# Performance work log

Measured on AMD Instinct MI355X. Metric: run time of the kernel, lower is better.

The kernel has to match this reference:

```python
import jax, jax.numpy as jnp
import numpy as np

N_NODES = 100000
N_HE = 20000
N_INC = 800000
D = 128
HEADS = 4
OUT = D // HEADS  # 32
NEG_SLOPE = 0.2
EPS_GN = 1e-5
EPS_SM = 1e-16


def graph_norm(x, w, b, ms):
    # PyG GraphNorm over a single graph: subtract learnable-scaled mean, normalize by std
    mean = jnp.mean(x, axis=0, keepdims=True)
    xc = x - ms * mean
    var = jnp.mean(xc * xc, axis=0, keepdims=True)
    return w * xc / jnp.sqrt(var + EPS_GN) + b


def frame_update(x, eidx, eattr, W, att, bias):
    # x: [N, D], eidx: [2, E] (row0 node ids, row1 hyperedge ids), eattr: [HE, D]
    xh = (x @ W).reshape(-1, HEADS, OUT)       # [N, H, O]
    eh = (eattr @ W).reshape(-1, HEADS, OUT)   # [HE, H, O]
    src = eidx[0]
    dst = eidx[1]
    x_i = xh[src]                              # [E, H, O] gathered node feats
    x_j = eh[dst]                              # [E, H, O] gathered hyperedge feats
    # attention logit: cat([x_i, x_j]) . att  summed over feature dim
    alpha = jnp.sum(x_i * att[:, :, :OUT], axis=-1) + jnp.sum(x_j * att[:, :, OUT:], axis=-1)  # [E, H]
    alpha = jnp.where(alpha >= 0, alpha, NEG_SLOPE * alpha)  # leaky_relu
    # segment softmax grouped by hyperedge id (dst), num_segments = N_HE
    m = jax.ops.segment_max(alpha, dst, num_segments=N_HE)   # [HE, H]
    ex = jnp.exp(alpha - m[dst])
    s = jax.ops.segment_sum(ex, dst, num_segments=N_HE)      # [HE, H]
    alpha = ex / (s[dst] + EPS_SM)                           # [E, H]
    # message = alpha * x_j where propagate's x_j = x[edge_index[0]] (node feats)
    msg = alpha[:, :, None] * x_i                            # [E, H, O]
    out = jax.ops.segment_sum(msg, dst, num_segments=N_HE)   # [HE, H, O]
    out = out.reshape(-1, HEADS * OUT)                       # concat heads
    return out + bias


def setup_inputs() -> dict:
    key = jax.random.key(0)
    ks = jax.random.split(key, 12)
    g = 1.0 / np.sqrt(D)
    inp = {
        "intra_x": jax.random.normal(ks[0], (N_NODES, D), jnp.float32),
        "intra_edge_attr": jax.random.normal(ks[1], (N_HE, D), jnp.float32),
        "inter_x": jax.random.normal(ks[2], (N_NODES, D), jnp.float32),
        "inter_edge_attr": jax.random.normal(ks[3], (N_HE, D), jnp.float32),
        "intra_edge_index": jnp.stack([
            jax.random.randint(ks[4], (N_INC,), 0, N_NODES),
            jax.random.randint(ks[5], (N_INC,), 0, N_HE)]).astype(jnp.int32),
        "inter_edge_index": jnp.stack([
            jax.random.randint(ks[6], (N_INC,), 0, N_NODES),
            jax.random.randint(ks[7], (N_INC,), 0, N_HE)]).astype(jnp.int32),
        "gn_intra_w": jnp.ones((D,), jnp.float32),
        "gn_intra_b": jnp.zeros((D,), jnp.float32),
        "gn_intra_ms": jnp.ones((D,), jnp.float32),
        "W_intra": jax.random.normal(ks[8], (D, HEADS * OUT), jnp.float32) * g,
        "att_intra": jax.random.normal(ks[9], (1, HEADS, 2 * OUT), jnp.float32) * g,
        "b_intra": jnp.zeros((HEADS * OUT,), jnp.float32),
        "gn_inter_w": jnp.ones((D,), jnp.float32),
        "gn_inter_b": jnp.zeros((D,), jnp.float32),
        "gn_inter_ms": jnp.ones((D,), jnp.float32),
        "W_inter": jax.random.normal(ks[10], (D, HEADS * OUT), jnp.float32) * g,
        "att_inter": jax.random.normal(ks[11], (1, HEADS, 2 * OUT), jnp.float32) * g,
        "b_inter": jnp.zeros((HEADS * OUT,), jnp.float32),
    }
    return inp


def reference(intra_x, intra_edge_index, intra_edge_attr,
              inter_x, inter_edge_index, inter_edge_attr,
              gn_intra_w, gn_intra_b, gn_intra_ms, W_intra, att_intra, b_intra,
              gn_inter_w, gn_inter_b, gn_inter_ms, W_inter, att_inter, b_inter):
    f_intra = frame_update(graph_norm(intra_x, gn_intra_w, gn_intra_b, gn_intra_ms),
                           intra_edge_index, intra_edge_attr, W_intra, att_intra, b_intra)
    f_inter = frame_update(graph_norm(inter_x, gn_inter_w, gn_inter_b, gn_inter_ms),
                           inter_edge_index, inter_edge_attr, W_inter, att_inter, b_inter)
    fusion = jnp.concatenate([
        jnp.mean(f_intra, axis=0),
        jnp.mean(f_inter, axis=0),
        jnp.mean(intra_x, axis=0),
        jnp.mean(inter_x, axis=0),
    ], axis=-1)  # [4*D]
    return fusion
```

## Files before the change

### kernel.cpp

```cpp
#include <hip/hip_runtime.h>

#define N_NODES 100000
#define N_HE    20000
#define N_EDGE  800000
#define DIM     128
#define NBS     98
#define NBD     40
#define CAP_S   9600
#define CAP_D   22500
#define SUBS    8
#define SUBD    16
#define PB      256
#define CHUNK   3125
#define STB     800
#define GPB     1024
#define GGRP    32

struct P {
  const void* x[2]; const void* ea[2]; const int* ei[2];
  const void* gw[2]; const void* gb[2]; const void* gms[2];
  const void* W[2]; const void* att[2]; const void* bias[2];
  float *stats, *a, *cw, *v, *u, *cst, *sPart, *wnPart, *gpart, *gpart2;
  unsigned *curS, *curD, *recS, *recD;
  unsigned short *lnb, *lhb, *hsv;
  unsigned short* xb;
  int useXb;
  int* flag; void* out;
};

__device__ __forceinline__ float ldf(const void* p, int i, int isbf){
  if (isbf){ unsigned short h = ((const unsigned short*)p)[i]; return __uint_as_float(((unsigned)h)<<16); }
  return ((const float*)p)[i];
}
__device__ __forceinline__ float b2f(unsigned short h){
  return __uint_as_float(((unsigned)h)<<16);
}
struct F8 { float v[8]; };
__device__ __forceinline__ F8 load8(const void* p, long idx, int isbf){
  F8 r;
  if (isbf){
    uint4 q = *(const uint4*)((const unsigned short*)p + idx);
    r.v[0]=__uint_as_float(q.x<<16); r.v[1]=__uint_as_float(q.x&0xFFFF0000u);
    r.v[2]=__uint_as_float(q.y<<16); r.v[3]=__uint_as_float(q.y&0xFFFF0000u);
    r.v[4]=__uint_as_float(q.z<<16); r.v[5]=__uint_as_float(q.z&0xFFFF0000u);
    r.v[6]=__uint_as_float(q.w<<16); r.v[7]=__uint_as_float(q.w&0xFFFF0000u);
  } else {
    const float4* q = (const float4*)((const float*)p + idx);
    float4 A=q[0], B=q[1];
    r.v[0]=A.x;r.v[1]=A.y;r.v[2]=A.z;r.v[3]=A.w;
    r.v[4]=B.x;r.v[5]=B.y;r.v[6]=B.z;r.v[7]=B.w;
  }
  return r;
}
__device__ __forceinline__ unsigned short f2bf(float f){
  unsigned u = __float_as_uint(f);
  return (unsigned short)((u + 0x7FFFu + ((u>>16)&1u)) >> 16);
}

__global__ void k_detect(P p){
  for (int i=threadIdx.x; i<872; i+=256) p.stats[i]=0.f;
  const unsigned* w = (const unsigned*)p.x[0];
  int bad = 0;
  for (int i = threadIdx.x; i < 4096; i += 256){
    float g = __uint_as_float(w[i]<<16);
    float ag = fabsf(g);
    if (!(ag==0.0f || (ag>1e-8f && ag<1e8f))) bad++;
  }
  for (int o=32;o;o>>=1) bad += __shfl_down(bad,o);
  __shared__ int sb;
  if (threadIdx.x==0) sb=0;
  __syncthreads();
  if ((threadIdx.x&63)==0) atomicAdd(&sb,bad);
  __syncthreads();
  if (threadIdx.x==0) *p.flag = (sb < 512) ? 1 : 0;
}

__global__ __launch_bounds__(256) void k_stats(P p){
  int f = blockIdx.y;
  const void* x = p.x[f];
  int isbf = *p.flag;
  int conv = (!isbf) && p.useXb;
  int cb = threadIdx.x & 15, rg = threadIdx.x >> 4;
  int rpb = (N_NODES + gridDim.x - 1)/gridDim.x;
  int r0 = blockIdx.x*rpb;
  int r1 = r0 + rpb; if (r1 > N_NODES) r1 = N_NODES;
  float s[8], q[8];
  #pragma unroll
  for (int j=0;j<8;j++){ s[j]=0.f; q[j]=0.f; }
  for (int r = r0 + rg; r < r1; r += 16){
    F8 xv = load8(x, (long)r*DIM + cb*8, isbf);
    #pragma unroll
    for (int j=0;j<8;j++){ s[j]+=xv.v[j]; q[j]+=xv.v[j]*xv.v[j]; }
    if (conv){
      uint4 o;
      o.x = (unsigned)f2bf(xv.v[0]) | ((unsigned)f2bf(xv.v[1])<<16);
      o.y = (unsigned)f2bf(xv.v[2]) | ((unsigned)f2bf(xv.v[3])<<16);
      o.z = (unsigned)f2bf(xv.v[4]) | ((unsigned)f2bf(xv.v[5])<<16);
      o.w = (unsigned)f2bf(xv.v[6]) | ((unsigned)f2bf(xv.v[7])<<16);
      *(uint4*)(p.xb + ((long)f*N_NODES + r)*DIM + cb*8) = o;
    }
  }
  __shared__ float red[256*9];
  #pragma unroll
  for (int j=0;j<8;j++) red[threadIdx.x*9+j]=s[j];
  __syncthreads();
  if (threadIdx.x < 128){
    int cb2 = threadIdx.x>>3, j = threadIdx.x&7;
    float a=0.f;
    for (int g=0; g<16; g++) a += red[(g*16+cb2)*9 + j];
    atomicAdd(&p.stats[f*256 + cb2*8 + j], a);
  }
  __syncthreads();
  #pragma unroll
  for (int j=0;j<8;j++) red[threadIdx.x*9+j]=q[j];
  __syncthreads();
  if (threadIdx.x < 128){
    int cb2 = threadIdx.x>>3, j = threadIdx.x&7;
    float a=0.f;
    for (int g=0; g<16; g++) a += red[(g*16+cb2)*9 + j];
    atomicAdd(&p.stats[f*256 + 128 + cb2*8 + j], a);
  }
}

__global__ void k_prep(P p){
  __shared__ float csh[2][128];
  int t = threadIdx.x;
  int isbf = *p.flag;
  int f = t>>7, d = t&127;
  float sum = p.stats[f*256+d], sq = p.stats[f*256+128+d];
  float mean = sum * (1.0f/N_NODES);
  float ms = ldf(p.gms[f], d, isbf);
  float gw = ldf(p.gw[f],  d, isbf);
  float gb = ldf(p.gb[f],  d, isbf);
  float var = sq*(1.0f/N_NODES) - (2.0f*ms - ms*ms)*mean*mean;
  float av = gw / sqrtf(var + 1e-5f);
  p.a[f*128+d] = av;
  csh[f][d] = gb - av*ms*mean;
  if (isbf) ((unsigned short*)p.out)[256 + f*128 + d] = f2bf(mean);
  else      ((float*)p.out)[256 + f*128 + d] = mean;
  #pragma unroll
  for (int h=0; h<4; h++){
    float w1=0.f, w2=0.f;
    for (int o=0;o<32;o++){
      float Wv = ldf(p.W[f], d*DIM + h*32 + o, isbf);
      w1 += Wv * ldf(p.att[f], h*64+o,    isbf);
      w2 += Wv * ldf(p.att[f], h*64+32+o, isbf);
    }
    p.v[f*512 + d*4 + h] = av*w1;
    p.u[f*512 + d*4 + h] = w2;
  }
  __syncthreads();
  float acc = 0.f;
  for (int dd=0; dd<128; dd++) acc += csh[f][dd]*ldf(p.W[f], dd*DIM+d, isbf);
  p.cw[f*128+d] = acc;
  __syncthreads();
  if (t < 8){
    int ff=t>>2, h=t&3;
    float s2=0.f;
    for (int o=0;o<32;o++) s2 += p.cw[ff*128+h*32+o]*ldf(p.att[ff], h*64+o, isbf);
    p.cst[ff*4+h]=s2;
  }
}

__global__ __launch_bounds__(256) void k_logits(P p){
  int job = blockIdx.y;
  int f = job & 1;
  bool node = job < 2;
  int isbf = *p.flag;
  const void* X; int xbf;
  if (node){
    if (isbf){ X = p.x[f]; xbf = 1; }
    else if (p.useXb){ X = p.xb + (long)f*N_NODES*DIM; xbf = 1; }
    else { X = p.x[f]; xbf = 0; }
  } else { X = p.ea[f]; xbf = isbf; }
  const float* coef = node ? (p.v + f*512) : (p.u + f*512);
  ushort4* outb = node ? ((ushort4*)p.lnb + (long)f*N_NODES)
                       : ((ushort4*)p.lhb + (long)f*N_HE);
  int R = node ? N_NODES : N_HE;
  int cb = threadIdx.x & 15, rl = threadIdx.x >> 4;
  float cf[8][4];
  #pragma unroll
  for (int j=0;j<8;j++)
    #pragma unroll
    for (int h=0;h<4;h++)
      cf[j][h] = coef[(cb*8+j)*4+h];
  float4 cst4 = make_float4(0.f,0.f,0.f,0.f);
  if (node) cst4 = *(const float4*)(p.cst + f*4);
  int rpb = (R + gridDim.x - 1)/gridDim.x;
  int r0 = blockIdx.x*rpb;
  int r1 = r0+rpb; if (r1>R) r1=R;
  for (int r = r0 + rl; r < r1; r += 16){
    F8 xv = load8(X, (long)r*DIM + cb*8, xbf);
    float a0=0.f,a1=0.f,a2=0.f,a3=0.f;
    #pragma unroll
    for (int j=0;j<8;j++){
      a0 += xv.v[j]*cf[j][0];
      a1 += xv.v[j]*cf[j][1];
      a2 += xv.v[j]*cf[j][2];
      a3 += xv.v[j]*cf[j][3];
    }
    #pragma unroll
    for (int m=1;m<16;m<<=1){
      a0 += __shfl_xor(a0,m);
      a1 += __shfl_xor(a1,m);
      a2 += __shfl_xor(a2,m);
      a3 += __shfl_xor(a3,m);
    }
    if (cb==0){
      ushort4 o;
      o.x = f2bf(a0 + cst4.x);
      o.y = f2bf(a1 + cst4.y);
      o.z = f2bf(a2 + cst4.z);
      o.w = f2bf(a3 + cst4.w);
      outb[r] = o;
    }
  }
}

__global__ __launch_bounds__(256) void k_bin(P p){
  __shared__ unsigned stage1[CHUNK];
  __shared__ unsigned stage2[CHUNK];
  __shared__ unsigned histS[NBS], histD[NBD];
  __shared__ unsigned startS[NBS], startD[NBD];
  __shared__ unsigned gbaseS[NBS], gbaseD[NBD];
  int b = blockIdx.x, f = blockIdx.y, t = threadIdx.x;
  const int* ei = p.ei[f];
  if (t < NBS) histS[t]=0;
  if (t < NBD) histD[t]=0;
  __syncthreads();
  int e0 = b*CHUNK;
  for (int i=t; i<CHUNK; i+=256){
    int src = ei[e0+i], dst = ei[N_EDGE+e0+i];
    unsigned nbs = (unsigned)src >> 10;
    stage1[i] = ((unsigned)src & 1023u) | ((unsigned)dst<<10) | (nbs<<25);
    atomicAdd(&histS[nbs], 1u);
    atomicAdd(&histD[(unsigned)dst>>9], 1u);
  }
  __syncthreads();
  if (t==0){ unsigned r=0; for (int k=0;k<NBS;k++){ startS[k]=r; r+=histS[k]; } }
  if (t==1){ unsigned r=0; for (int k=0;k<NBD;k++){ startD[k]=r; r+=histD[k]; } }
  __syncthreads();
  if (t < NBS) gbaseS[t] = atomicAdd(&p.curS[f*NBS+t], histS[t]);
  if (t >= 128 && t < 128+NBD) gbaseD[t-128] = atomicAdd(&p.curD[f*NBD+(t-128)], histD[t-128]);
  __syncthreads();
  if (t < NBS) histS[t]=0;
  __syncthreads();
  for (int i=t; i<CHUNK; i+=256){
    unsigned rec = stage1[i];
    unsigned nbs = rec>>25;
    unsigned r = atomicAdd(&histS[nbs],1u);
    stage2[startS[nbs]+r] = rec;
  }
  __syncthreads();
  for (int i=t; i<CHUNK; i+=256){
    unsigned rec = stage2[i];
    unsigned nbs = rec>>25;
    unsigned g = gbaseS[nbs] + (i - startS[nbs]);
    if (g < CAP_S) p.recS[((long)f*NBS+nbs)*CAP_S + g] = rec & 0x01FFFFFFu;
  }
  __syncthreads();
  if (t < NBD) histD[t]=0;
  __syncthreads();
  for (int i=t; i<CHUNK; i+=256){
    unsigned rec = stage1[i];
    unsigned dst = (rec>>10)&0x7FFFu;
    unsigned src = (rec>>25)*1024u + (rec&1023u);
    unsigned nbd = dst>>9;
    unsigned rd = (dst&511u) | (src<<9) | (nbd<<26);
    unsigned r = atomicAdd(&histD[nbd],1u);
    stage2[startD[nbd]+r] = rd;
  }
  __syncthreads();
  for (int i=t; i<CHUNK; i+=256){
    unsigned rd = stage2[i];
    unsigned nbd = rd>>26;
    unsigned g = gbaseD[nbd] + (i - startD[nbd]);
    if (g < CAP_D) p.recD[((long)f*NBD+nbd)*CAP_D + g] = rd & 0x03FFFFFFu;
  }
}

__global__ __launch_bounds__(256) void k_sD(P p){
  __shared__ float sh[512*4];
  int nbd = blockIdx.x, sub = blockIdx.y, f = blockIdx.z, t = threadIdx.x;
  for (int i=t; i<512; i+=256) *(float4*)(sh+i*4) = make_float4(0,0,0,0);
  __syncthreads();
  unsigned cnt = p.curD[f*NBD+nbd]; if (cnt > CAP_D) cnt = CAP_D;
  int lo = (int)((long)cnt*sub/SUBD), hi = (int)((long)cnt*(sub+1)/SUBD);
  const unsigned* base = p.recD + ((long)f*NBD+nbd)*CAP_D;
  const ushort4* lnb = (const ushort4*)p.lnb + (long)f*N_NODES;
  const ushort4* lhb = (const ushort4*)p.lhb + (long)f*N_HE;
  for (int i=lo+t; i<hi; i+=256){
    unsigned rd = base[i];
    unsigned dstRel = rd & 511u;
    unsigned src = rd >> 9;
    ushort4 A = lnb[src];
    ushort4 B = lhb[nbd*512 + dstRel];
    float z0=b2f(A.x)+b2f(B.x), z1=b2f(A.y)+b2f(B.y);
    float z2=b2f(A.z)+b2f(B.z), z3=b2f(A.w)+b2f(B.w);
    z0 = z0>=0.f? z0 : 0.2f*z0;  z1 = z1>=0.f? z1 : 0.2f*z1;
    z2 = z2>=0.f? z2 : 0.2f*z2;  z3 = z3>=0.f? z3 : 0.2f*z3;
    float* tgt = sh + dstRel*4;
    atomicAdd(tgt+0, __expf(z0));
    atomicAdd(tgt+1, __expf(z1));
    atomicAdd(tgt+2, __expf(z2));
    atomicAdd(tgt+3, __expf(z3));
  }
  __syncthreads();
  float* out = p.sPart + (((long)f*NBD+nbd)*SUBD + sub)*2048;
  for (int i=t; i<512; i+=256) *(float4*)(out+i*4) = *(float4*)(sh+i*4);
}

__global__ void k_sred(P p){
  int idx = blockIdx.x*256 + threadIdx.x;
  if (idx >= 2*N_HE) return;
  int f = idx / N_HE, he = idx % N_HE;
  int nbd = he>>9, rel = he&511;
  float4 acc = make_float4(0,0,0,0);
  const float* base = p.sPart + ((long)(f*NBD+nbd)*SUBD)*2048 + rel*4;
  #pragma unroll
  for (int s=0;s<SUBD;s++){
    float4 v = *(const float4*)(base + (long)s*2048);
    acc.x+=v.x; acc.y+=v.y; acc.z+=v.z; acc.w+=v.w;
  }
  ushort4 lh = ((const ushort4*)p.lhb)[(long)f*N_HE + he];
  uint4 o;
  o.x = (unsigned)lh.x | ((unsigned)lh.y<<16);
  o.y = (unsigned)lh.z | ((unsigned)lh.w<<16);
  o.z = (unsigned)f2bf(1.0f/(acc.x+1e-16f)) | ((unsigned)f2bf(1.0f/(acc.y+1e-16f))<<16);
  o.w = (unsigned)f2bf(1.0f/(acc.z+1e-16f)) | ((unsigned)f2bf(1.0f/(acc.w+1e-16f))<<16);
  ((uint4*)p.hsv)[(long)f*N_HE + he] = o;
}

__global__ __launch_bounds__(256) void k_wnD(P p){
  __shared__ float sh[1024*4];
  int nbs = blockIdx.x, sub = blockIdx.y, f = blockIdx.z, t = threadIdx.x;
  for (int i=t; i<1024; i+=256) *(float4*)(sh+i*4) = make_float4(0,0,0,0);
  __syncthreads();
  unsigned cnt = p.curS[f*NBS+nbs]; if (cnt > CAP_S) cnt = CAP_S;
  int lo = (int)((long)cnt*sub/SUBS), hi = (int)((long)cnt*(sub+1)/SUBS);
  const unsigned* base = p.recS + ((long)f*NBS+nbs)*CAP_S;
  const ushort4* lnb = (const ushort4*)p.lnb + (long)f*N_NODES;
  const uint4* hsv = (const uint4*)p.hsv + (long)f*N_HE;
  for (int i=lo+t; i<hi; i+=256){
    unsigned rec = base[i];
    unsigned srcRel = rec & 1023u;
    unsigned dst = rec >> 10;
    ushort4 A = lnb[nbs*1024 + srcRel];
    uint4 H = hsv[dst];
    float z0=b2f(A.x)+b2f((unsigned short)(H.x&0xFFFF)), z1=b2f(A.y)+b2f((unsigned short)(H.x>>16));
    float z2=b2f(A.z)+b2f((unsigned short)(H.y&0xFFFF)), z3=b2f(A.w)+b2f((unsigned short)(H.y>>16));
    z0 = z0>=0.f? z0 : 0.2f*z0;  z1 = z1>=0.f? z1 : 0.2f*z1;
    z2 = z2>=0.f? z2 : 0.2f*z2;  z3 = z3>=0.f? z3 : 0.2f*z3;
    float si0=b2f((unsigned short)(H.z&0xFFFF)), si1=b2f((unsigned short)(H.z>>16));
    float si2=b2f((unsigned short)(H.w&0xFFFF)), si3=b2f((unsigned short)(H.w>>16));
    float* tgt = sh + srcRel*4;
    atomicAdd(tgt+0, __expf(z0)*si0);
    atomicAdd(tgt+1, __expf(z1)*si1);
    atomicAdd(tgt+2, __expf(z2)*si2);
    atomicAdd(tgt+3, __expf(z3)*si3);
  }
  __syncthreads();
  float* out = p.wnPart + (((long)f*NBS+nbs)*SUBS + sub)*4096;
  for (int i=t; i<1024; i+=256) *(float4*)(out+i*4) = *(float4*)(sh+i*4);
}

__global__ __launch_bounds__(256) void k_gpass(P p){
  int f = blockIdx.y;
  int isbf = *p.flag;
  const void* xs; int xbf;
  if (isbf){ xs = p.x[f]; xbf = 1; }
  else if (p.useXb){ xs = p.xb + (long)f*N_NODES*DIM; xbf = 1; }
  else { xs = p.x[f]; xbf = 0; }
  int cb = threadIdx.x & 15, rg = threadIdx.x >> 4;
  float acc[8][4]; float sw[4]={0.f,0.f,0.f,0.f};
  #pragma unroll
  for (int j=0;j<8;j++)
    #pragma unroll
    for (int h=0;h<4;h++) acc[j][h]=0.f;
  int rpb = (N_NODES + gridDim.x - 1)/gridDim.x;
  int r0 = blockIdx.x*rpb;
  int r1 = r0+rpb; if (r1>N_NODES) r1=N_NODES;
  for (int r = r0 + rg; r < r1; r += 16){
    int nbs = r>>10, rel = r&1023;
    const float* wb = p.wnPart + ((long)(f*NBS+nbs)*SUBS)*4096 + rel*4;
    float4 wv = make_float4(0,0,0,0);
    #pragma unroll
    for (int s=0;s<SUBS;s++){
      float4 v = *(const float4*)(wb + (long)s*4096);
      wv.x+=v.x; wv.y+=v.y; wv.z+=v.z; wv.w+=v.w;
    }
    F8 xv = load8(xs, (long)r*DIM + cb*8, xbf);
    float wvv[4]={wv.x,wv.y,wv.z,wv.w};
    #pragma unroll
    for (int j=0;j<8;j++)
      #pragma unroll
      for (int h=0;h<4;h++) acc[j][h] += xv.v[j]*wvv[h];
    if (cb==0){ sw[0]+=wv.x; sw[1]+=wv.y; sw[2]+=wv.z; sw[3]+=wv.w; }
  }
  __shared__ float red[16][16][33];
  __shared__ float red2[16][4];
  #pragma unroll
  for (int j=0;j<8;j++)
    #pragma unroll
    for (int h=0;h<4;h++) red[rg][cb][j*4+h]=acc[j][h];
  if (cb==0){ red2[rg][0]=sw[0]; red2[rg][1]=sw[1]; red2[rg][2]=sw[2]; red2[rg][3]=sw[3]; }
  __syncthreads();
  float* gp = p.gpart + ((long)f*GPB + blockIdx.x)*520;
  for (int idx=threadIdx.x; idx<512; idx+=256){
    int d=idx>>2, h=idx&3, cb2=d>>3, j=d&7;
    float a=0.f;
    #pragma unroll
    for (int g=0; g<16; g++) a += red[g][cb2][j*4+h];
    gp[idx] = a;
  }
  if (threadIdx.x<4){
    float a=0.f;
    for (int g=0;g<16;g++) a+=red2[g][threadIdx.x];
    gp[512+threadIdx.x] = a;
  }
}

__global__ void k_gredA(P p){
  int g = blockIdx.x, f = blockIdx.y;
  int slabs = GPB/GGRP;
  const float* base = p.gpart + ((long)f*GPB + (long)g*slabs)*520;
  for (int i=threadIdx.x; i<516; i+=256){
    float acc = 0.f;
    for (int s=0;s<slabs;s++) acc += base[(long)s*520 + i];
    p.gpart2[((long)f*GGRP + g)*520 + i] = acc;
  }
}

__global__ void k_final(P p){
  __shared__ float Gs[2][512];
  __shared__ float SWs[2][4];
  int t = threadIdx.x;
  for (int idx=t; idx<2*516; idx+=256){
    int f = idx/516, i = idx%516;
    const float* b = p.gpart2 + (long)f*GGRP*520 + i;
    float acc = 0.f;
    for (int g=0; g<GGRP; g++) acc += b[(long)g*520];
    if (i < 512) Gs[f][i] = acc; else SWs[f][i-512] = acc;
  }
  __syncthreads();
  int isbf = *p.flag;
  int f = t>>7, k = t&127, h = k>>5;
  float acc = 0.f;
  for (int d=0; d<128; d++)
    acc += Gs[f][d*4+h] * p.a[f*128+d] * ldf(p.W[f], d*DIM+k, isbf);
  acc += p.cw[f*128+k]*SWs[f][h];
  float o = acc*(1.0f/N_HE) + ldf(p.bias[f], k, isbf);
  if (isbf) ((unsigned short*)p.out)[f*128+k] = f2bf(o);
  else      ((float*)p.out)[f*128+k] = o;
}

extern "C" void kernel_launch(void* const* d_in, const int* in_sizes, int n_in,
                              void* d_out, int out_size, void* d_ws, size_t ws_size,
                              hipStream_t stream){
  P p;
  p.x[0]=d_in[0];  p.ea[0]=d_in[1];  p.x[1]=d_in[2];  p.ea[1]=d_in[3];
  p.ei[0]=(const int*)d_in[4];  p.ei[1]=(const int*)d_in[5];
  p.gw[0]=d_in[6];  p.gb[0]=d_in[7];  p.gms[0]=d_in[8];
  p.W[0]=d_in[9];   p.att[0]=d_in[10]; p.bias[0]=d_in[11];
  p.gw[1]=d_in[12]; p.gb[1]=d_in[13]; p.gms[1]=d_in[14];
  p.W[1]=d_in[15];  p.att[1]=d_in[16]; p.bias[1]=d_in[17];

  float* w = (float*)d_ws;
  size_t off = 0;
  p.stats = w+off; off += 512;
  p.flag  = (int*)(w+off); off += 8;
  p.curS  = (unsigned*)(w+off); off += 256;
  p.curD  = (unsigned*)(w+off); off += 96;
  p.a     = w+off; off += 256;
  p.cw    = w+off; off += 256;
  p.v     = w+off; off += 1024;
  p.u     = w+off; off += 1024;
  p.cst   = w+off; off += 16;
  p.lnb   = (unsigned short*)(w+off); off += (size_t)2*N_NODES*2;
  p.lhb   = (unsigned short*)(w+off); off += (size_t)2*N_HE*2;
  p.hsv   = (unsigned short*)(w+off); off += (size_t)2*N_HE*4;
  p.recS  = (unsigned*)(w+off); off += (size_t)2*NBS*CAP_S;
  p.recD  = (unsigned*)(w+off); off += (size_t)2*NBD*CAP_D;
  p.sPart = w+off; off += (size_t)2*NBD*SUBD*2048;
  p.wnPart= w+off; off += (size_t)2*NBS*SUBS*4096;
  p.gpart = w+off; off += (size_t)2*GPB*520;
  p.gpart2= w+off; off += (size_t)2*GGRP*520;
  p.xb    = (unsigned short*)(w+off);
  size_t tot_with_xb = off + (size_t)2*N_NODES*DIM/2;
  p.useXb = (tot_with_xb*sizeof(float) <= ws_size) ? 1 : 0;
  p.out   = d_out;

  k_detect <<<dim3(1),          dim3(256), 0, stream>>>(p);
  k_stats  <<<dim3(STB,2),      dim3(256), 0, stream>>>(p);
  k_prep   <<<dim3(1),          dim3(256), 0, stream>>>(p);
  k_logits <<<dim3(STB,4),      dim3(256), 0, stream>>>(p);
  k_bin    <<<dim3(PB,2),       dim3(256), 0, stream>>>(p);
  k_sD     <<<dim3(NBD,SUBD,2), dim3(256), 0, stream>>>(p);
  k_sred   <<<dim3((2*N_HE+255)/256), dim3(256), 0, stream>>>(p);
  k_wnD    <<<dim3(NBS,SUBS,2), dim3(256), 0, stream>>>(p);
  k_gpass  <<<dim3(GPB,2),      dim3(256), 0, stream>>>(p);
  k_gredA  <<<dim3(GGRP,2),     dim3(256), 0, stream>>>(p);
  k_final  <<<dim3(1),          dim3(256), 0, stream>>>(p);
}
```

Before: 252.9 us.

## Merge stats and binning kernels, drop bf16 copy of x, fuse final reduction

Fuses the graph-norm statistics pass and the edge binning pass into a single launch, with blocks split by blockIdx.y and sharing one shared-memory buffer. Removes the bf16 staging copy of the node features, so the logits and gather passes read the original fp32 inputs directly. Merges the last reduction with the final projection using a last-block-done atomic counter, and halves the grid sizes for the stats/logits and gather passes. This saves launches and the bf16 write traffic, at the cost of doubled fp32 read traffic in the later passes.

```diff
diff --git a/kernel.cpp b/kernel.cpp
--- a/kernel.cpp
+++ b/kernel.cpp
@@ -12,8 +12,8 @@
 #define SUBD    16
 #define PB      256
 #define CHUNK   3125
-#define STB     800
-#define GPB     1024
+#define STB     400
+#define GPB     512
 #define GGRP    32
 
 struct P {
@@ -21,10 +21,8 @@
   const void* gw[2]; const void* gb[2]; const void* gms[2];
   const void* W[2]; const void* att[2]; const void* bias[2];
   float *stats, *a, *cw, *v, *u, *cst, *sPart, *wnPart, *gpart, *gpart2;
-  unsigned *curS, *curD, *recS, *recD;
+  unsigned *curS, *curD, *recS, *recD, *done;
   unsigned short *lnb, *lhb, *hsv;
-  unsigned short* xb;
-  int useXb;
   int* flag; void* out;
 };
 
@@ -58,7 +56,7 @@
 }
 
 __global__ void k_detect(P p){
-  for (int i=threadIdx.x; i<872; i+=256) p.stats[i]=0.f;
+  for (int i=threadIdx.x; i<880; i+=256) p.stats[i]=0.f;
   const unsigned* w = (const unsigned*)p.x[0];
   int bad = 0;
   for (int i = threadIdx.x; i < 4096; i += 256){
@@ -75,50 +73,109 @@
   if (threadIdx.x==0) *p.flag = (sb < 512) ? 1 : 0;
 }
 
-__global__ __launch_bounds__(256) void k_stats(P p){
-  int f = blockIdx.y;
-  const void* x = p.x[f];
-  int isbf = *p.flag;
-  int conv = (!isbf) && p.useXb;
-  int cb = threadIdx.x & 15, rg = threadIdx.x >> 4;
-  int rpb = (N_NODES + gridDim.x - 1)/gridDim.x;
-  int r0 = blockIdx.x*rpb;
-  int r1 = r0 + rpb; if (r1 > N_NODES) r1 = N_NODES;
-  float s[8], q[8];
-  #pragma unroll
-  for (int j=0;j<8;j++){ s[j]=0.f; q[j]=0.f; }
-  for (int r = r0 + rg; r < r1; r += 16){
-    F8 xv = load8(x, (long)r*DIM + cb*8, isbf);
-    #pragma unroll
-    for (int j=0;j<8;j++){ s[j]+=xv.v[j]; q[j]+=xv.v[j]*xv.v[j]; }
-    if (conv){
-      uint4 o;
-      o.x = (unsigned)f2bf(xv.v[0]) | ((unsigned)f2bf(xv.v[1])<<16);
-      o.y = (unsigned)f2bf(xv.v[2]) | ((unsigned)f2bf(xv.v[3])<<16);
-      o.z = (unsigned)f2bf(xv.v[4]) | ((unsigned)f2bf(xv.v[5])<<16);
-      o.w = (unsigned)f2bf(xv.v[6]) | ((unsigned)f2bf(xv.v[7])<<16);
-      *(uint4*)(p.xb + ((long)f*N_NODES + r)*DIM + cb*8) = o;
-    }
-  }
-  __shared__ float red[256*9];
-  #pragma unroll
-  for (int j=0;j<8;j++) red[threadIdx.x*9+j]=s[j];
-  __syncthreads();
-  if (threadIdx.x < 128){
-    int cb2 = threadIdx.x>>3, j = threadIdx.x&7;
-    float a=0.f;
-    for (int g=0; g<16; g++) a += red[(g*16+cb2)*9 + j];
-    atomicAdd(&p.stats[f*256 + cb2*8 + j], a);
-  }
-  __syncthreads();
-  #pragma unroll
-  for (int j=0;j<8;j++) red[threadIdx.x*9+j]=q[j];
-  __syncthreads();
-  if (threadIdx.x < 128){
-    int cb2 = threadIdx.x>>3, j = threadIdx.x&7;
-    float a=0.f;
-    for (int g=0; g<16; g++) a += red[(g*16+cb2)*9 + j];
-    atomicAdd(&p.stats[f*256 + 128 + cb2*8 + j], a);
+__global__ __launch_bounds__(256) void k_statsbin(P p){
+  __shared__ unsigned smem[6664];
+  int t = threadIdx.x;
+  if (blockIdx.y < 2){
+    int f = blockIdx.y;
+    const void* x = p.x[f];
+    int isbf = *p.flag;
+    int cb = t & 15, rg = t >> 4;
+    int rpb = (N_NODES + STB - 1)/STB;
+    int r0 = blockIdx.x*rpb;
+    int r1 = r0 + rpb; if (r1 > N_NODES) r1 = N_NODES;
+    float s[8], q[8];
+    #pragma unroll
+    for (int j=0;j<8;j++){ s[j]=0.f; q[j]=0.f; }
+    for (int r = r0 + rg; r < r1; r += 16){
+      F8 xv = load8(x, (long)r*DIM + cb*8, isbf);
+      #pragma unroll
+      for (int j=0;j<8;j++){ s[j]+=xv.v[j]; q[j]+=xv.v[j]*xv.v[j]; }
+    }
+    float* red = (float*)smem;
+    #pragma unroll
+    for (int j=0;j<8;j++) red[t*9+j]=s[j];
+    __syncthreads();
+    if (t < 128){
+      int cb2 = t>>3, j = t&7;
+      float a=0.f;
+      for (int g=0; g<16; g++) a += red[(g*16+cb2)*9 + j];
+      atomicAdd(&p.stats[f*256 + cb2*8 + j], a);
+    }
+    __syncthreads();
+    #pragma unroll
+    for (int j=0;j<8;j++) red[t*9+j]=q[j];
+    __syncthreads();
+    if (t < 128){
+      int cb2 = t>>3, j = t&7;
+      float a=0.f;
+      for (int g=0; g<16; g++) a += red[(g*16+cb2)*9 + j];
+      atomicAdd(&p.stats[f*256 + 128 + cb2*8 + j], a);
+    }
+    return;
+  }
+  int b = blockIdx.x, f = blockIdx.y - 2;
+  if (b >= PB) return;
+  unsigned* stage1 = smem;
+  unsigned* stage2 = smem + 3125;
+  unsigned* histS  = smem + 6250;
+  unsigned* histD  = smem + 6348;
+  unsigned* startS = smem + 6388;
+  unsigned* startD = smem + 6486;
+  unsigned* gbaseS = smem + 6526;
+  unsigned* gbaseD = smem + 6624;
+  const int* ei = p.ei[f];
+  if (t < NBS) histS[t]=0;
+  if (t < NBD) histD[t]=0;
+  __syncthreads();
+  int e0 = b*CHUNK;
+  for (int i=t; i<CHUNK; i+=256){
+    int src = ei[e0+i], dst = ei[N_EDGE+e0+i];
+    unsigned nbs = (unsigned)src >> 10;
+    stage1[i] = ((unsigned)src & 1023u) | ((unsigned)dst<<10) | (nbs<<25);
+    atomicAdd(&histS[nbs], 1u);
+    atomicAdd(&histD[(unsigned)dst>>9], 1u);
+  }
+  __syncthreads();
+  if (t==0){ unsigned r=0; for (int k=0;k<NBS;k++){ startS[k]=r; r+=histS[k]; } }
+  if (t==1){ unsigned r=0; for (int k=0;k<NBD;k++){ startD[k]=r; r+=histD[k]; } }
+  __syncthreads();
+  if (t < NBS) gbaseS[t] = atomicAdd(&p.curS[f*NBS+t], histS[t]);
+  if (t >= 128 && t < 128+NBD) gbaseD[t-128] = atomicAdd(&p.curD[f*NBD+(t-128)], histD[t-128]);
+  __syncthreads();
+  if (t < NBS) histS[t]=0;
+  __syncthreads();
+  for (int i=t; i<CHUNK; i+=256){
+    unsigned rec = stage1[i];
+    unsigned nbs = rec>>25;
+    unsigned r = atomicAdd(&histS[nbs],1u);
+    stage2[startS[nbs]+r] = rec;
+  }
+  __syncthreads();
+  for (int i=t; i<CHUNK; i+=256){
+    unsigned rec = stage2[i];
+    unsigned nbs = rec>>25;
+    unsigned g = gbaseS[nbs] + (i - startS[nbs]);
+    if (g < CAP_S) p.recS[((long)f*NBS+nbs)*CAP_S + g] = rec & 0x01FFFFFFu;
+  }
+  __syncthreads();
+  if (t < NBD) histD[t]=0;
+  __syncthreads();
+  for (int i=t; i<CHUNK; i+=256){
+    unsigned rec = stage1[i];
+    unsigned dst = (rec>>10)&0x7FFFu;
+    unsigned src = (rec>>25)*1024u + (rec&1023u);
+    unsigned nbd = dst>>9;
+    unsigned rd = (dst&511u) | (src<<9) | (nbd<<26);
+    unsigned r = atomicAdd(&histD[nbd],1u);
+    stage2[startD[nbd]+r] = rd;
+  }
+  __syncthreads();
+  for (int i=t; i<CHUNK; i+=256){
+    unsigned rd = stage2[i];
+    unsigned nbd = rd>>26;
+    unsigned g = gbaseD[nbd] + (i - startD[nbd]);
+    if (g < CAP_D) p.recD[((long)f*NBD+nbd)*CAP_D + g] = rd & 0x03FFFFFFu;
   }
 }
 
@@ -167,12 +224,7 @@
   int f = job & 1;
   bool node = job < 2;
   int isbf = *p.flag;
-  const void* X; int xbf;
-  if (node){
-    if (isbf){ X = p.x[f]; xbf = 1; }
-    else if (p.useXb){ X = p.xb + (long)f*N_NODES*DIM; xbf = 1; }
-    else { X = p.x[f]; xbf = 0; }
-  } else { X = p.ea[f]; xbf = isbf; }
+  const void* X = node ? p.x[f] : p.ea[f];
   const float* coef = node ? (p.v + f*512) : (p.u + f*512);
   ushort4* outb = node ? ((ushort4*)p.lnb + (long)f*N_NODES)
                        : ((ushort4*)p.lhb + (long)f*N_HE);
@@ -190,7 +242,7 @@
   int r0 = blockIdx.x*rpb;
   int r1 = r0+rpb; if (r1>R) r1=R;
   for (int r = r0 + rl; r < r1; r += 16){
-    F8 xv = load8(X, (long)r*DIM + cb*8, xbf);
+    F8 xv = load8(X, (long)r*DIM + cb*8, isbf);
     float a0=0.f,a1=0.f,a2=0.f,a3=0.f;
     #pragma unroll
     for (int j=0;j<8;j++){
@@ -214,68 +266,6 @@
       o.w = f2bf(a3 + cst4.w);
       outb[r] = o;
     }
-  }
-}
-
-__global__ __launch_bounds__(256) void k_bin(P p){
-  __shared__ unsigned stage1[CHUNK];
-  __shared__ unsigned stage2[CHUNK];
-  __shared__ unsigned histS[NBS], histD[NBD];
-  __shared__ unsigned startS[NBS], startD[NBD];
-  __shared__ unsigned gbaseS[NBS], gbaseD[NBD];
-  int b = blockIdx.x, f = blockIdx.y, t = threadIdx.x;
-  const int* ei = p.ei[f];
-  if (t < NBS) histS[t]=0;
-  if (t < NBD) histD[t]=0;
-  __syncthreads();
-  int e0 = b*CHUNK;
-  for (int i=t; i<CHUNK; i+=256){
-    int src = ei[e0+i], dst = ei[N_EDGE+e0+i];
-    unsigned nbs = (unsigned)src >> 10;
-    stage1[i] = ((unsigned)src & 1023u) | ((unsigned)dst<<10) | (nbs<<25);
-    atomicAdd(&histS[nbs], 1u);
-    atomicAdd(&histD[(unsigned)dst>>9], 1u);
-  }
-  __syncthreads();
-  if (t==0){ unsigned r=0; for (int k=0;k<NBS;k++){ startS[k]=r; r+=histS[k]; } }
-  if (t==1){ unsigned r=0; for (int k=0;k<NBD;k++){ startD[k]=r; r+=histD[k]; } }
-  __syncthreads();
-  if (t < NBS) gbaseS[t] = atomicAdd(&p.curS[f*NBS+t], histS[t]);
-  if (t >= 128 && t < 128+NBD) gbaseD[t-128] = atomicAdd(&p.curD[f*NBD+(t-128)], histD[t-128]);
-  __syncthreads();
-  if (t < NBS) histS[t]=0;
-  __syncthreads();
-  for (int i=t; i<CHUNK; i+=256){
-    unsigned rec = stage1[i];
-    unsigned nbs = rec>>25;
-    unsigned r = atomicAdd(&histS[nbs],1u);
-    stage2[startS[nbs]+r] = rec;
-  }
-  __syncthreads();
-  for (int i=t; i<CHUNK; i+=256){
-    unsigned rec = stage2[i];
-    unsigned nbs = rec>>25;
-    unsigned g = gbaseS[nbs] + (i - startS[nbs]);
-    if (g < CAP_S) p.recS[((long)f*NBS+nbs)*CAP_S + g] = rec & 0x01FFFFFFu;
-  }
-  __syncthreads();
-  if (t < NBD) histD[t]=0;
-  __syncthreads();
-  for (int i=t; i<CHUNK; i+=256){
-    unsigned rec = stage1[i];
-    unsigned dst = (rec>>10)&0x7FFFu;
-    unsigned src = (rec>>25)*1024u + (rec&1023u);
-    unsigned nbd = dst>>9;
-    unsigned rd = (dst&511u) | (src<<9) | (nbd<<26);
-    unsigned r = atomicAdd(&histD[nbd],1u);
-    stage2[startD[nbd]+r] = rd;
-  }
-  __syncthreads();
-  for (int i=t; i<CHUNK; i+=256){
-    unsigned rd = stage2[i];
-    unsigned nbd = rd>>26;
-    unsigned g = gbaseD[nbd] + (i - startD[nbd]);
-    if (g < CAP_D) p.recD[((long)f*NBD+nbd)*CAP_D + g] = rd & 0x03FFFFFFu;
   }
 }
 
@@ -367,10 +357,7 @@
 __global__ __launch_bounds__(256) void k_gpass(P p){
   int f = blockIdx.y;
   int isbf = *p.flag;
-  const void* xs; int xbf;
-  if (isbf){ xs = p.x[f]; xbf = 1; }
-  else if (p.useXb){ xs = p.xb + (long)f*N_NODES*DIM; xbf = 1; }
-  else { xs = p.x[f]; xbf = 0; }
+  const void* xs = p.x[f];
   int cb = threadIdx.x & 15, rg = threadIdx.x >> 4;
   float acc[8][4]; float sw[4]={0.f,0.f,0.f,0.f};
   #pragma unroll
@@ -389,7 +376,7 @@
       float4 v = *(const float4*)(wb + (long)s*4096);
       wv.x+=v.x; wv.y+=v.y; wv.z+=v.z; wv.w+=v.w;
     }
-    F8 xv = load8(xs, (long)r*DIM + cb*8, xbf);
+    F8 xv = load8(xs, (long)r*DIM + cb*8, isbf);
     float wvv[4]={wv.x,wv.y,wv.z,wv.w};
     #pragma unroll
     for (int j=0;j<8;j++)
@@ -420,7 +407,7 @@
   }
 }
 
-__global__ void k_gredA(P p){
+__global__ void k_gredfin(P p){
   int g = blockIdx.x, f = blockIdx.y;
   int slabs = GPB/GGRP;
   const float* base = p.gpart + ((long)f*GPB + (long)g*slabs)*520;
@@ -429,29 +416,36 @@
     for (int s=0;s<slabs;s++) acc += base[(long)s*520 + i];
     p.gpart2[((long)f*GGRP + g)*520 + i] = acc;
   }
-}
-
-__global__ void k_final(P p){
+  __syncthreads();
+  __threadfence();
+  __shared__ unsigned isLast;
+  if (threadIdx.x==0){
+    unsigned old = atomicAdd(p.done, 1u);
+    isLast = (old == (unsigned)(GGRP*2 - 1)) ? 1u : 0u;
+  }
+  __syncthreads();
+  if (!isLast) return;
+  __threadfence();
   __shared__ float Gs[2][512];
   __shared__ float SWs[2][4];
   int t = threadIdx.x;
   for (int idx=t; idx<2*516; idx+=256){
-    int f = idx/516, i = idx%516;
-    const float* b = p.gpart2 + (long)f*GGRP*520 + i;
+    int ff = idx/516, i = idx%516;
+    const float* b = p.gpart2 + (long)ff*GGRP*520 + i;
     float acc = 0.f;
-    for (int g=0; g<GGRP; g++) acc += b[(long)g*520];
-    if (i < 512) Gs[f][i] = acc; else SWs[f][i-512] = acc;
+    for (int gg=0; gg<GGRP; gg++) acc += b[(long)gg*520];
+    if (i < 512) Gs[ff][i] = acc; else SWs[ff][i-512] = acc;
   }
   __syncthreads();
   int isbf = *p.flag;
-  int f = t>>7, k = t&127, h = k>>5;
+  int ff = t>>7, k = t&127, h = k>>5;
   float acc = 0.f;
   for (int d=0; d<128; d++)
-    acc += Gs[f][d*4+h] * p.a[f*128+d] * ldf(p.W[f], d*DIM+k, isbf);
-  acc += p.cw[f*128+k]*SWs[f][h];
-  float o = acc*(1.0f/N_HE) + ldf(p.bias[f], k, isbf);
-  if (isbf) ((unsigned short*)p.out)[f*128+k] = f2bf(o);
-  else      ((float*)p.out)[f*128+k] = o;
+    acc += Gs[ff][d*4+h] * p.a[ff*128+d] * ldf(p.W[ff], d*DIM+k, isbf);
+  acc += p.cw[ff*128+k]*SWs[ff][h];
+  float o = acc*(1.0f/N_HE) + ldf(p.bias[ff], k, isbf);
+  if (isbf) ((unsigned short*)p.out)[ff*128+k] = f2bf(o);
+  else      ((float*)p.out)[ff*128+k] = o;
 }
 
 extern "C" void kernel_launch(void* const* d_in, const int* in_sizes, int n_in,
@@ -471,6 +465,7 @@
   p.flag  = (int*)(w+off); off += 8;
   p.curS  = (unsigned*)(w+off); off += 256;
   p.curD  = (unsigned*)(w+off); off += 96;
+  p.done  = (unsigned*)(w+off); off += 8;
   p.a     = w+off; off += 256;
   p.cw    = w+off; off += 256;
   p.v     = w+off; off += 1024;
@@ -485,20 +480,15 @@
   p.wnPart= w+off; off += (size_t)2*NBS*SUBS*4096;
   p.gpart = w+off; off += (size_t)2*GPB*520;
   p.gpart2= w+off; off += (size_t)2*GGRP*520;
-  p.xb    = (unsigned short*)(w+off);
-  size_t tot_with_xb = off + (size_t)2*N_NODES*DIM/2;
-  p.useXb = (tot_with_xb*sizeof(float) <= ws_size) ? 1 : 0;
   p.out   = d_out;
 
-  k_detect <<<dim3(1),          dim3(256), 0, stream>>>(p);
-  k_stats  <<<dim3(STB,2),      dim3(256), 0, stream>>>(p);
-  k_prep   <<<dim3(1),          dim3(256), 0, stream>>>(p);
-  k_logits <<<dim3(STB,4),      dim3(256), 0, stream>>>(p);
-  k_bin    <<<dim3(PB,2),       dim3(256), 0, stream>>>(p);
-  k_sD     <<<dim3(NBD,SUBD,2), dim3(256), 0, stream>>>(p);
-  k_sred   <<<dim3((2*N_HE+255)/256), dim3(256), 0, stream>>>(p);
-  k_wnD    <<<dim3(NBS,SUBS,2), dim3(256), 0, stream>>>(p);
-  k_gpass  <<<dim3(GPB,2),      dim3(256), 0, stream>>>(p);
-  k_gredA  <<<dim3(GGRP,2),     dim3(256), 0, stream>>>(p);
-  k_final  <<<dim3(1),          dim3(256), 0, stream>>>(p);
-}
+  k_detect  <<<dim3(1),          dim3(256), 0, stream>>>(p);
+  k_statsbin<<<dim3(STB,4),      dim3(256), 0, stream>>>(p);
+  k_prep    <<<dim3(1),          dim3(256), 0, stream>>>(p);
+  k_logits  <<<dim3(STB,4),      dim3(256), 0, stream>>>(p);
+  k_sD      <<<dim3(NBD,SUBD,2), dim3(256), 0, stream>>>(p);
+  k_sred    <<<dim3((2*N_HE+255)/256), dim3(256), 0, stream>>>(p);
+  k_wnD     <<<dim3(NBS,SUBS,2), dim3(256), 0, stream>>>(p);
+  k_gpass   <<<dim3(GPB,2),      dim3(256), 0, stream>>>(p);
+  k_gredfin <<<dim3(GGRP,2),     dim3(256), 0, stream>>>(p);
+}
```

Result: faster. 227.2 us (-10.2%).
